# Kernel optimization log

Measured on AMD Instinct MI355X. Metric: run time of the kernel, lower is better.

## Reference

```python
import jax, jax.numpy as jnp
import numpy as np


def setup_inputs() -> dict:
    key = jax.random.key(0)
    k1, k2, k3 = jax.random.split(key, 3)
    T, H, E = 16384, 4096, 64  # tokens, hidden_size, num_experts
    x = jax.random.normal(k1, (T, H), dtype=jnp.float32)
    weight = jax.random.normal(k2, (E, H), dtype=jnp.float32) * (1.0 / np.sqrt(H))
    bias = jax.random.normal(k3, (E,), dtype=jnp.float32) * 0.01
    return {"x": x, "weight": weight, "bias": bias}


def reference(x, weight, bias):
    TOP_K = 8
    # logits: [T, E] = x @ weight.T + bias
    logits = jnp.einsum("th,eh->te", x, weight) + bias
    top_values, top_indices = jax.lax.top_k(logits, TOP_K)  # [T, K]
    top_weights = jax.nn.softmax(top_values, axis=-1)
    return (top_weights, top_indices)
```

## Files before the change

kernel.cpp:

```cpp
#include <hip/hip_runtime.h>
#include <float.h>
#include <math.h>

#define TOKS 16384
#define HDIM 4096
#define NEXP 64
#define BM   64
#define NTILE (TOKS / BM)
#define KS   4
#define NCHS 16
#define WPE  262144

typedef __attribute__((ext_vector_type(8)))  short short8v;
typedef __attribute__((ext_vector_type(16))) float f32x16;

__device__ __forceinline__ void split3(float v, unsigned& b1, unsigned& b2, unsigned& b3) {
  unsigned xb = __float_as_uint(v);
  b1 = xb >> 16;
  float r = v - __uint_as_float(xb & 0xFFFF0000u);
  unsigned rb = __float_as_uint(r);
  b2 = rb >> 16;
  float r2 = r - __uint_as_float(rb & 0xFFFF0000u);
  b3 = __float_as_uint(r2) >> 16;
}
__device__ __forceinline__ void cvt2(float a, float b, unsigned& o1, unsigned& o2, unsigned& o3) {
  unsigned a1, a2, a3, c1, c2, c3;
  split3(a, a1, a2, a3);
  split3(b, c1, c2, c3);
  o1 = a1 | (c1 << 16); o2 = a2 | (c2 << 16); o3 = a3 | (c3 << 16);
}

__global__ __launch_bounds__(256)
void wsplit_kernel(const float* __restrict__ wgt, unsigned short* __restrict__ wsp) {
  const int gid  = blockIdx.x * 256 + threadIdx.x;
  const int base = gid * 8;
  const float4 f0 = *(const float4*)(wgt + base);
  const float4 f1 = *(const float4*)(wgt + base + 4);
  uint4 q1, q2, q3;
  cvt2(f0.x, f0.y, q1.x, q2.x, q3.x);
  cvt2(f0.z, f0.w, q1.y, q2.y, q3.y);
  cvt2(f1.x, f1.y, q1.z, q2.z, q3.z);
  cvt2(f1.z, f1.w, q1.w, q2.w, q3.w);
  *(uint4*)(wsp + base)            = q1;
  *(uint4*)(wsp + WPE + base)      = q2;
  *(uint4*)(wsp + 2 * WPE + base)  = q3;
}

__device__ __forceinline__ void gload_lds16(const float* g, void* l) {
  __builtin_amdgcn_global_load_lds((const __attribute__((address_space(1))) void*)g,
                                   (__attribute__((address_space(3))) void*)l, 16, 0, 0);
}

#define WAITVM(N) do { asm volatile("s_waitcnt vmcnt(" #N ")" ::: "memory"); \
                       __builtin_amdgcn_sched_barrier(0); } while (0)
#define RBAR()    do { __builtin_amdgcn_s_barrier(); \
                       __builtin_amdgcn_sched_barrier(0); } while (0)

__global__ __launch_bounds__(256)
void router_mfma_kernel(const float* __restrict__ x,
                        const unsigned short* __restrict__ wsp,
                        float* __restrict__ part) {
  __shared__ __align__(16) unsigned char smem[49152];
  const int tid  = threadIdx.x;
  const int lane = tid & 63;
  const int wv   = tid >> 6;
  const int kt   = blockIdx.y;
  const int tokBase = blockIdx.x * BM;
  const int kStart  = kt * (HDIM / KS);

  const float* xg[4];
#pragma unroll
  for (int j = 0; j < 4; ++j) {
    const unsigned G = j * 256 + tid;
    const unsigned g = G ^ ((G >> 4) & 7);
    xg[j] = x + (size_t)(tokBase + (g >> 4)) * HDIM + kStart + (g & 15) * 4;
  }
  const int ldsb = wv * 1024;

  const int wm = wv >> 1, we = wv & 1;
  const int r  = lane & 31, h2 = lane >> 5;
  const int rowA = wm * 32 + r;
  const int r7A  = rowA & 7;
  const unsigned short* const bp = wsp + (size_t)(we * 32 + r) * HDIM + kStart + h2 * 8;

  f32x16 m0, m1, c0, c1, c2;
#pragma unroll
  for (int i = 0; i < 16; ++i) { m0[i] = 0.f; m1[i] = 0.f; c0[i] = 0.f; c1[i] = 0.f; c2[i] = 0.f; }

#define STAGE(buf, c) do { \
    unsigned char* lb_ = smem + (buf) * 16384; \
    gload_lds16(xg[0] + (c) * 64, lb_ +     0 + ldsb); \
    gload_lds16(xg[1] + (c) * 64, lb_ +  4096 + ldsb); \
    gload_lds16(xg[2] + (c) * 64, lb_ +  8192 + ldsb); \
    gload_lds16(xg[3] + (c) * 64, lb_ + 12288 + ldsb); \
  } while (0)

#define MFMA(a, b, c) __builtin_amdgcn_mfma_f32_32x32x16_bf16((a), (b), (c), 0, 0, 0)

#define COMPUTE(buf, c) do { \
    const unsigned char* bb_ = smem + (buf) * 16384; \
    _Pragma("unroll") \
    for (int s = 0; s < 4; ++s) { \
      const unsigned g0_ = rowA * 16 + s * 4 + h2 * 2; \
      const float4 xlo_ = *(const float4*)(bb_ + ((g0_ ^ r7A) << 4)); \
      const float4 xhi_ = *(const float4*)(bb_ + (((g0_ + 1) ^ r7A) << 4)); \
      uint4 q1_, q2_, q3_; \
      cvt2(xlo_.x, xlo_.y, q1_.x, q2_.x, q3_.x); \
      cvt2(xlo_.z, xlo_.w, q1_.y, q2_.y, q3_.y); \
      cvt2(xhi_.x, xhi_.y, q1_.z, q2_.z, q3_.z); \
      cvt2(xhi_.z, xhi_.w, q1_.w, q2_.w, q3_.w); \
      const short8v a1_ = __builtin_bit_cast(short8v, q1_); \
      const short8v a2_ = __builtin_bit_cast(short8v, q2_); \
      const short8v a3_ = __builtin_bit_cast(short8v, q3_); \
      const unsigned short* bq_ = bp + (c) * 64 + s * 16; \
      const short8v b1_ = *(const short8v*)(bq_); \
      const short8v b2_ = *(const short8v*)(bq_ + WPE); \
      const short8v b3_ = *(const short8v*)(bq_ + 2 * WPE); \
      if (s < 2) m0 = MFMA(a1_, b1_, m0); \
      else       m1 = MFMA(a1_, b1_, m1); \
      c0 = MFMA(a1_, b2_, c0); \
      c1 = MFMA(a2_, b1_, c1); \
      c2 = MFMA(a1_, b3_, c2); \
      c0 = MFMA(a2_, b2_, c0); \
      c1 = MFMA(a3_, b1_, c1); \
    } \
  } while (0)

  STAGE(0, 0);
  STAGE(1, 1);
  STAGE(2, 2);
  WAITVM(8);
  RBAR();

#pragma unroll 1
  for (int c = 0; c < NCHS; ++c) {
    COMPUTE(c % 3, c);
    RBAR();
    if (c + 3 < NCHS) STAGE(c % 3, c + 3);
    if (c + 3 < NCHS)      { WAITVM(8); }
    else if (c + 2 < NCHS) { WAITVM(4); }
    else if (c + 1 < NCHS) { WAITVM(0); }
    if (c + 1 < NCHS) RBAR();
  }

  float* pp = part + ((size_t)kt * NTILE + blockIdx.x) * 4096;
#pragma unroll
  for (int reg = 0; reg < 16; ++reg) {
    const int rowf = (reg & 3) + 8 * (reg >> 2) + 4 * h2;
    pp[(wm * 32 + rowf) * 64 + we * 32 + r] =
        ((m0[reg] + m1[reg]) + (c0[reg] + c1[reg])) + c2[reg];
  }
}

__global__ __launch_bounds__(64)
void reduce_topk_kernel(const float* __restrict__ part,
                        const float* __restrict__ bias,
                        float* __restrict__ out) {
  __shared__ __align__(16) float fin[1024];
  const int lane = threadIdx.x;
  const int g    = blockIdx.x;
  const int tile = g >> 2;
  const int rowBase = (g & 3) * 16;

  const int row = lane >> 2;
  const int e0  = (lane & 3) * 16;
  const size_t off0 = (size_t)tile * 4096 + (rowBase + row) * 64 + e0;
  float4 s0 = make_float4(0.f, 0.f, 0.f, 0.f), s1 = s0, s2 = s0, s3 = s0;
#pragma unroll
  for (int kt = 0; kt < KS; ++kt) {
    const float* p = part + (size_t)kt * (NTILE * 4096) + off0;
    const float4 q0 = *(const float4*)(p);
    const float4 q1 = *(const float4*)(p + 4);
    const float4 q2 = *(const float4*)(p + 8);
    const float4 q3 = *(const float4*)(p + 12);
    s0.x += q0.x; s0.y += q0.y; s0.z += q0.z; s0.w += q0.w;
    s1.x += q1.x; s1.y += q1.y; s1.z += q1.z; s1.w += q1.w;
    s2.x += q2.x; s2.y += q2.y; s2.z += q2.z; s2.w += q2.w;
    s3.x += q3.x; s3.y += q3.y; s3.z += q3.z; s3.w += q3.w;
  }
  *(float4*)(&fin[lane * 16])      = s0;
  *(float4*)(&fin[lane * 16 + 4])  = s1;
  *(float4*)(&fin[lane * 16 + 8])  = s2;
  *(float4*)(&fin[lane * 16 + 12]) = s3;
  __syncthreads();

  for (int tt = 0; tt < 16; ++tt) {
    float v = fin[tt * 64 + lane] + bias[lane];
    float myval = 0.f, m0 = 0.f;
    int myidx = 0;
#pragma unroll
    for (int k = 0; k < 8; ++k) {
      float bv = v;
      int   bi = lane;
#pragma unroll
      for (int off = 1; off < 64; off <<= 1) {
        const float ov = __shfl_xor(bv, off);
        const int   oi = __shfl_xor(bi, off);
        if (ov > bv || (ov == bv && oi < bi)) { bv = ov; bi = oi; }
      }
      if (k == 0) m0 = bv;
      if (lane == k) { myval = bv; myidx = bi; }
      if (lane == bi) v = -FLT_MAX;
    }
    const float el = (lane < 8) ? expf(myval - m0) : 0.f;
    float ssum = el;
    ssum += __shfl_xor(ssum, 1);
    ssum += __shfl_xor(ssum, 2);
    ssum += __shfl_xor(ssum, 4);
    if (lane < 8) {
      const size_t tg = (size_t)g * 16 + tt;
      out[tg * 8 + lane] = el / ssum;
      out[(size_t)TOKS * 8 + tg * 8 + lane] = (float)myidx;
    }
  }
}

extern "C" void kernel_launch(void* const* d_in, const int* in_sizes, int n_in,
                              void* d_out, int out_size, void* d_ws, size_t ws_size,
                              hipStream_t stream) {
  const float* x    = (const float*)d_in[0];
  const float* wgt  = (const float*)d_in[1];
  const float* bias = (const float*)d_in[2];
  float* out  = (float*)d_out;
  float* part = (float*)d_ws;

  unsigned short* wsp = (unsigned short*)((char*)d_ws + (size_t)KS * NTILE * 4096 * sizeof(float));

  hipLaunchKernelGGL(wsplit_kernel, dim3(NEXP * HDIM / (256 * 8)), dim3(256), 0, stream,
                     wgt, wsp);
  hipLaunchKernelGGL(router_mfma_kernel, dim3(NTILE, KS), dim3(256), 0, stream,
                     x, wsp, part);
  hipLaunchKernelGGL(reduce_topk_kernel, dim3(TOKS / 16), dim3(64), 0, stream,
                     part, bias, out);
}
```

Before: 197.0 us.

## Stage split weights through LDS, double-buffer, and double the K-split

The bf16x3 split weight operand is now staged into shared memory with async global-to-LDS loads alongside x, instead of each wave reading it directly from global memory. The pipeline moves from a triple buffer of 64-wide K chunks to a double buffer of 32-wide chunks, and the K-split doubles from 4 to 8 so more blocks are in flight. The aim is to cut redundant global weight traffic and raise occupancy. The cost is twice as many partial sums for the reduce kernel to read, shallower prefetch, and one fewer accumulator (the c2 terms are folded into c0 and c1).

```diff
diff --git a/kernel.cpp b/kernel.cpp
--- a/kernel.cpp
+++ b/kernel.cpp
@@ -7,8 +7,9 @@
 #define NEXP 64
 #define BM   64
 #define NTILE (TOKS / BM)
-#define KS   4
+#define KS   8
 #define NCHS 16
+#define BK   32
 #define WPE  262144
 
 typedef __attribute__((ext_vector_type(8)))  short short8v;
@@ -46,7 +47,7 @@
   *(uint4*)(wsp + 2 * WPE + base)  = q3;
 }
 
-__device__ __forceinline__ void gload_lds16(const float* g, void* l) {
+__device__ __forceinline__ void gload_lds16(const void* g, void* l) {
   __builtin_amdgcn_global_load_lds((const __attribute__((address_space(1))) void*)g,
                                    (__attribute__((address_space(3))) void*)l, 16, 0, 0);
 }
@@ -60,7 +61,7 @@
 void router_mfma_kernel(const float* __restrict__ x,
                         const unsigned short* __restrict__ wsp,
                         float* __restrict__ part) {
-  __shared__ __align__(16) unsigned char smem[49152];
+  __shared__ __align__(16) unsigned char smem[40960];
   const int tid  = threadIdx.x;
   const int lane = tid & 63;
   const int wv   = tid >> 6;
@@ -68,42 +69,45 @@
   const int tokBase = blockIdx.x * BM;
   const int kStart  = kt * (HDIM / KS);
 
-  const float* xg[4];
-#pragma unroll
-  for (int j = 0; j < 4; ++j) {
-    const unsigned G = j * 256 + tid;
-    const unsigned g = G ^ ((G >> 4) & 7);
-    xg[j] = x + (size_t)(tokBase + (g >> 4)) * HDIM + kStart + (g & 15) * 4;
-  }
-  const int ldsb = wv * 1024;
+  const int arow = wv * 16 + (lane >> 3);
+  const int aq   = (lane & 7) ^ (lane >> 3);
+  const float* const asrc0 = x + (size_t)(tokBase + arow) * HDIM + kStart + aq * 4;
+  const float* const asrc1 = asrc0 + (size_t)8 * HDIM;
+  const int brow = wv * 16 + (lane >> 2);
+  const int bq   = (lane & 3) ^ ((lane >> 2) & 3);
+  const unsigned short* const bsrc0 = wsp +           (size_t)brow * HDIM + kStart + bq * 8;
+  const unsigned short* const bsrc1 = bsrc0 + WPE;
+  const unsigned short* const bsrc2 = bsrc0 + 2 * WPE;
 
   const int wm = wv >> 1, we = wv & 1;
   const int r  = lane & 31, h2 = lane >> 5;
-  const int rowA = wm * 32 + r;
-  const int r7A  = rowA & 7;
-  const unsigned short* const bp = wsp + (size_t)(we * 32 + r) * HDIM + kStart + h2 * 8;
-
-  f32x16 m0, m1, c0, c1, c2;
-#pragma unroll
-  for (int i = 0; i < 16; ++i) { m0[i] = 0.f; m1[i] = 0.f; c0[i] = 0.f; c1[i] = 0.f; c2[i] = 0.f; }
+  const int rA = wm * 32 + r;     const int r7A = rA & 7;
+  const int rB = we * 32 + r;     const int r3B = rB & 3;
+
+  f32x16 m0, m1, c0, c1;
+#pragma unroll
+  for (int i = 0; i < 16; ++i) { m0[i] = 0.f; m1[i] = 0.f; c0[i] = 0.f; c1[i] = 0.f; }
 
 #define STAGE(buf, c) do { \
-    unsigned char* lb_ = smem + (buf) * 16384; \
-    gload_lds16(xg[0] + (c) * 64, lb_ +     0 + ldsb); \
-    gload_lds16(xg[1] + (c) * 64, lb_ +  4096 + ldsb); \
-    gload_lds16(xg[2] + (c) * 64, lb_ +  8192 + ldsb); \
-    gload_lds16(xg[3] + (c) * 64, lb_ + 12288 + ldsb); \
+    unsigned char* lb_ = smem + (buf) * 20480; \
+    const int kc_ = (c) * BK; \
+    gload_lds16(asrc0 + kc_, lb_ + wv * 2048); \
+    gload_lds16(asrc1 + kc_, lb_ + wv * 2048 + 1024); \
+    gload_lds16(bsrc0 + kc_, lb_ + 8192 + wv * 1024); \
+    gload_lds16(bsrc1 + kc_, lb_ + 8192 + (wv + 4) * 1024); \
+    gload_lds16(bsrc2 + kc_, lb_ + 8192 + (wv + 8) * 1024); \
   } while (0)
 
 #define MFMA(a, b, c) __builtin_amdgcn_mfma_f32_32x32x16_bf16((a), (b), (c), 0, 0, 0)
 
-#define COMPUTE(buf, c) do { \
-    const unsigned char* bb_ = smem + (buf) * 16384; \
+#define COMPUTE(buf) do { \
+    const unsigned char* ab_ = smem + (buf) * 20480; \
+    const unsigned char* bb_ = ab_ + 8192; \
     _Pragma("unroll") \
-    for (int s = 0; s < 4; ++s) { \
-      const unsigned g0_ = rowA * 16 + s * 4 + h2 * 2; \
-      const float4 xlo_ = *(const float4*)(bb_ + ((g0_ ^ r7A) << 4)); \
-      const float4 xhi_ = *(const float4*)(bb_ + (((g0_ + 1) ^ r7A) << 4)); \
+    for (int s = 0; s < 2; ++s) { \
+      const int qa_ = s * 4 + h2 * 2; \
+      const float4 xlo_ = *(const float4*)(ab_ + rA * 128 + (( qa_      ^ r7A) << 4)); \
+      const float4 xhi_ = *(const float4*)(ab_ + rA * 128 + (((qa_ + 1) ^ r7A) << 4)); \
       uint4 q1_, q2_, q3_; \
       cvt2(xlo_.x, xlo_.y, q1_.x, q2_.x, q3_.x); \
       cvt2(xlo_.z, xlo_.w, q1_.y, q2_.y, q3_.y); \
@@ -112,43 +116,43 @@
       const short8v a1_ = __builtin_bit_cast(short8v, q1_); \
       const short8v a2_ = __builtin_bit_cast(short8v, q2_); \
       const short8v a3_ = __builtin_bit_cast(short8v, q3_); \
-      const unsigned short* bq_ = bp + (c) * 64 + s * 16; \
-      const short8v b1_ = *(const short8v*)(bq_); \
-      const short8v b2_ = *(const short8v*)(bq_ + WPE); \
-      const short8v b3_ = *(const short8v*)(bq_ + 2 * WPE); \
-      if (s < 2) m0 = MFMA(a1_, b1_, m0); \
-      else       m1 = MFMA(a1_, b1_, m1); \
+      const int qb_ = ((s * 2 + h2) ^ r3B) << 4; \
+      const short8v b1_ = *(const short8v*)(bb_ +        rB * 64 + qb_); \
+      const short8v b2_ = *(const short8v*)(bb_ + 4096 + rB * 64 + qb_); \
+      const short8v b3_ = *(const short8v*)(bb_ + 8192 + rB * 64 + qb_); \
+      if (s == 0) m0 = MFMA(a1_, b1_, m0); \
+      else        m1 = MFMA(a1_, b1_, m1); \
       c0 = MFMA(a1_, b2_, c0); \
       c1 = MFMA(a2_, b1_, c1); \
-      c2 = MFMA(a1_, b3_, c2); \
-      c0 = MFMA(a2_, b2_, c0); \
-      c1 = MFMA(a3_, b1_, c1); \
+      c0 = MFMA(a1_, b3_, c0); \
+      c1 = MFMA(a2_, b2_, c1); \
+      c0 = MFMA(a3_, b1_, c0); \
     } \
   } while (0)
 
   STAGE(0, 0);
   STAGE(1, 1);
-  STAGE(2, 2);
-  WAITVM(8);
+  WAITVM(5);
   RBAR();
-
 #pragma unroll 1
   for (int c = 0; c < NCHS; ++c) {
-    COMPUTE(c % 3, c);
+    COMPUTE(c & 1);
     RBAR();
-    if (c + 3 < NCHS) STAGE(c % 3, c + 3);
-    if (c + 3 < NCHS)      { WAITVM(8); }
-    else if (c + 2 < NCHS) { WAITVM(4); }
-    else if (c + 1 < NCHS) { WAITVM(0); }
-    if (c + 1 < NCHS) RBAR();
+    if (c + 2 < NCHS) {
+      STAGE(c & 1, c + 2);
+      WAITVM(5);
+      RBAR();
+    } else if (c + 1 < NCHS) {
+      WAITVM(0);
+      RBAR();
+    }
   }
 
   float* pp = part + ((size_t)kt * NTILE + blockIdx.x) * 4096;
 #pragma unroll
   for (int reg = 0; reg < 16; ++reg) {
     const int rowf = (reg & 3) + 8 * (reg >> 2) + 4 * h2;
-    pp[(wm * 32 + rowf) * 64 + we * 32 + r] =
-        ((m0[reg] + m1[reg]) + (c0[reg] + c1[reg])) + c2[reg];
+    pp[(wm * 32 + rowf) * 64 + we * 32 + r] = (m0[reg] + m1[reg]) + (c0[reg] + c1[reg]);
   }
 }
 
```

New measurement: 173.0 us. -12.2%, faster.
